# Kernel tuning notes

Hardware: AMD Instinct MI355X
Metric: run time of the kernel (lower is better)

## Reference

```python
import jax, jax.numpy as jnp
import numpy as np

B, T = 16, 2048
P_DIM = 512
NC = 8          # num_codebooks
CS = 256        # codebook_size
HD = 256        # hidden_dim (must equal CS, see module structure)
TOT = NC * CS   # 2048
SELF_OUT = (NC - 1) * HD
SELF_IN = (NC - 1) * CS
EPS = 1e-5


def setup_inputs() -> dict:
    key = jax.random.key(0)
    ks = jax.random.split(key, 6)
    predictor = jax.random.normal(ks[0], (B, T, P_DIM), dtype=jnp.float32)
    codebook_indexes = jax.random.randint(ks[1], (B, T, NC), 0, CS, dtype=jnp.int32)
    # linear1: predictor_dim -> NC*HD
    W1 = jax.random.normal(ks[2], (NC * HD, P_DIM), dtype=jnp.float32) * P_DIM ** -0.5
    b1 = jnp.zeros((NC * HD,), jnp.float32)
    # linear_self parameter, init as in the module
    linear_self = jax.random.normal(ks[3], (SELF_OUT, SELF_IN), dtype=jnp.float32) * SELF_IN ** -0.5
    # LayerNorm affine params
    gamma = jnp.ones((TOT,), jnp.float32)
    beta = jnp.zeros((TOT,), jnp.float32)
    # linear2: NC*HD -> NC*CS
    W2 = jax.random.normal(ks[4], (TOT, NC * HD), dtype=jnp.float32) * (NC * HD) ** -0.5
    b2 = jnp.zeros((TOT,), jnp.float32)
    return {"predictor": predictor, "codebook_indexes": codebook_indexes,
            "W1": W1, "b1": b1, "linear_self": linear_self,
            "gamma": gamma, "beta": beta, "W2": W2, "b2": b2}


def _self_mask():
    # block lower-triangular (inclusive) mask: out block i sees in blocks <= i
    oi = jnp.arange(SELF_OUT) // HD
    ii = jnp.arange(SELF_IN) // CS
    return (oi[:, None] >= ii[None, :]).astype(jnp.float32)


def reference(predictor, codebook_indexes, W1, b1, linear_self, gamma, beta, W2, b2):
    idx = codebook_indexes.astype(jnp.int32)
    N = idx.shape[0] * idx.shape[1]
    idx_f = idx.reshape(N, NC)
    pred_f = predictor.reshape(N, P_DIM)

    cb_mask = idx_f >= 0                                   # [N, NC]
    idx_floor = jnp.maximum(idx_f, 0)
    # scatter one-hot exactly as torch scatter_ (no per-codebook offset)
    one_hot = jnp.zeros((N, TOT), jnp.float32).at[
        jnp.arange(N)[:, None], idx_floor].set(cb_mask.astype(jnp.float32))

    one_hot_part = one_hot[:, : TOT - CS]                  # [N, (NC-1)*CS]
    W_self = linear_self * _self_mask()                    # [(NC-1)*HD, (NC-1)*CS]
    self_pred = one_hot_part @ W_self.T                    # [N, (NC-1)*HD]

    hidden = pred_f @ W1.T + b1                            # [N, NC*HD]
    hidden = hidden.at[:, CS:].add(self_pred)

    h = jax.nn.relu(hidden)
    mu = jnp.mean(h, axis=-1, keepdims=True)
    var = jnp.mean(jnp.square(h - mu), axis=-1, keepdims=True)
    h = (h - mu) * jax.lax.rsqrt(var + EPS) * gamma + beta

    logits = h @ W2.T + b2                                 # [N, TOT]
    logprobs = jax.nn.log_softmax(logits.reshape(N, NC, CS), axis=-1).reshape(N, TOT)

    tot_logprob = jnp.vdot(logprobs, one_hot)
    tot_count = jnp.sum(cb_mask)
    return tot_logprob, tot_count
```

## Files before the change

kernel.cpp:

```cpp
#include <hip/hip_runtime.h>

#define NROWS 32768
#define PD    512
#define NCB   8
#define CSZ   256
#define TOTD  2048
#define SIN   1792

typedef float floatx4  __attribute__((ext_vector_type(4)));
typedef float floatx16 __attribute__((ext_vector_type(16)));
typedef int   intx4    __attribute__((ext_vector_type(4)));
typedef int   intx8    __attribute__((ext_vector_type(8)));

__device__ __forceinline__ float bf2f(unsigned int h) {
    return __uint_as_float(h << 16);
}
__device__ __forceinline__ unsigned short f2bf(float f) {
    unsigned int u = __float_as_uint(f);
    u += 0x7FFFu + ((u >> 16) & 1u);
    return (unsigned short)(u >> 16);
}
__device__ __forceinline__ unsigned char f2fp8(float v) {
    int p = __builtin_amdgcn_cvt_pk_fp8_f32(v, v, 0, false);
    return (unsigned char)(p & 0xFF);
}

__device__ __forceinline__ void gload16(const unsigned char* g, unsigned char* l) {
    __builtin_amdgcn_global_load_lds(
        (const __attribute__((address_space(1))) void*)g,
        (__attribute__((address_space(3))) void*)l, 16, 0, 0);
}

#define MFMA64(ACC, A, B)                                                     \
    asm volatile("v_mfma_f32_32x32x64_f8f6f4 %0, %1, %2, %0"                  \
                 : "+a"(ACC) : "v"(A), "v"(B))

__global__ __launch_bounds__(256) void k_cvt8(const float* __restrict__ in,
                                              unsigned char* __restrict__ out,
                                              float scale, int n8) {
    int i = blockIdx.x * 256 + threadIdx.x;
    if (i >= n8) return;
    float4 a = ((const float4*)in)[2 * i];
    float4 b = ((const float4*)in)[2 * i + 1];
    int p0 = __builtin_amdgcn_cvt_pk_fp8_f32(a.x * scale, a.y * scale, 0, false);
    p0     = __builtin_amdgcn_cvt_pk_fp8_f32(a.z * scale, a.w * scale, p0, true);
    int p1 = __builtin_amdgcn_cvt_pk_fp8_f32(b.x * scale, b.y * scale, 0, false);
    p1     = __builtin_amdgcn_cvt_pk_fp8_f32(b.z * scale, b.w * scale, p1, true);
    int2 o; o.x = p0; o.y = p1;
    ((int2*)out)[i] = o;
}

__global__ __launch_bounds__(256) void k_tb(const float* __restrict__ in,
                                            unsigned short* __restrict__ out) {
    __shared__ float t[32][33];
    int bx = blockIdx.x * 32, by = blockIdx.y * 32;
    int tx = threadIdx.x & 31, ty = threadIdx.x >> 5;
#pragma unroll
    for (int j = 0; j < 32; j += 8)
        t[ty + j][tx] = in[(size_t)(by + ty + j) * SIN + bx + tx];
    __syncthreads();
#pragma unroll
    for (int j = 0; j < 32; j += 8)
        out[(size_t)(bx + ty + j) * SIN + by + tx] = f2bf(t[tx][ty + j]);
}


__global__ __launch_bounds__(512)
void k_gemm1(const unsigned char* __restrict__ A,
             const unsigned char* __restrict__ Bw,
             const float* __restrict__ bias,
             unsigned char* __restrict__ Out) {
    const int K = PD;
    __shared__ __align__(16) unsigned char As[3 * 8192];
    __shared__ __align__(16) unsigned char Bs[3 * 8192];

    const int tid  = threadIdx.x;
    const int lane = tid & 63;
    const int wave = tid >> 6;
    const int wm = (wave >> 2) << 6;
    const int wn = (wave & 3) << 5;
    const int bid  = blockIdx.x;
    const int row0 = (bid & 255) << 7;
    const int col0 = (bid >> 8) << 7;

    floatx16 acc0 = 0.f, acc1 = 0.f;

    const int gran  = lane >> 1;
    const int srow  = ((wave >> 1) << 5) + (gran ^ ((gran & 12) >> 2));
    const int skoff = ((wave & 1) << 5) + ((lane & 1) << 4);
    const unsigned char* Ag = A  + (size_t)(row0 + srow) * K + skoff;
    const unsigned char* Bg = Bw + (size_t)(col0 + srow) * K + skoff;
    unsigned char* Al = As + wave * 1024;
    unsigned char* Bl = Bs + wave * 1024;

    gload16(Ag,      Al);
    gload16(Bg,      Bl);
    gload16(Ag + 64, Al + 8192);
    gload16(Bg + 64, Bl + 8192);

    const int ro = (lane << 5) ^ ((lane & 12) << 3);
    const int aoff = (wave >> 2) << 12;
    const int boff = (wave & 3) << 11;

    auto compute = [&](int cbuf) {
        const unsigned char* Ab = As + cbuf * 8192 + aoff + ro;
        const unsigned char* Bb = Bs + cbuf * 8192 + boff + ro;
        intx8 a0 = *(const intx8*)Ab;
        intx8 a1 = *(const intx8*)(Ab + 2048);
        intx8 b0 = *(const intx8*)Bb;
        MFMA64(acc0, a0, b0);
        MFMA64(acc1, a1, b0);
    };

    const int NI = K / 64;
    int cb = 0, nb = 2;
    for (int i = 0; i < NI - 1; ++i) {
        asm volatile("s_waitcnt vmcnt(2)" ::: "memory");
        asm volatile("s_barrier" ::: "memory");
        if (i + 2 < NI) {
            const int k0 = (i + 2) * 64;
            gload16(Ag + k0, Al + nb * 8192);
            gload16(Bg + k0, Bl + nb * 8192);
        }
        compute(cb);
        cb = (cb + 1 == 3) ? 0 : cb + 1;
        nb = (nb + 1 == 3) ? 0 : nb + 1;
    }
    asm volatile("s_waitcnt vmcnt(0)" ::: "memory");
    asm volatile("s_barrier" ::: "memory");
    compute(cb);
    asm volatile("s_nop 7\n\ts_nop 7\n\ts_nop 7" ::: "memory");

    const int l31  = lane & 31;
    const int half = lane >> 5;
    const int col  = col0 + wn + l31;
    const float bcol = bias[col];
#pragma unroll
    for (int r = 0; r < 16; ++r) {
        const int rl = (r & 3) + ((r >> 2) << 3) + (half << 2);
        Out[(size_t)(row0 + wm + rl) * TOTD + col]      = f2fp8((acc0[r] * 0.0625f + bcol) * 8.f);
        Out[(size_t)(row0 + wm + 32 + rl) * TOTD + col] = f2fp8((acc1[r] * 0.0625f + bcol) * 8.f);
    }
}

__global__ __launch_bounds__(256) void k_ln(const unsigned char* __restrict__ Hraw8,
                                            unsigned char* __restrict__ H8,
                                            const unsigned short* __restrict__ LSTb,
                                            const int* __restrict__ idx,
                                            const float* __restrict__ gamma,
                                            const float* __restrict__ beta) {
    const int row = blockIdx.x;
    const int tid = threadIdx.x;
    __shared__ int sidx[8];
    __shared__ float ws4[4], wss4[4];
    if (tid < 8) sidx[tid] = idx[(size_t)row * NCB + tid];

    uint2 w = ((const uint2*)(Hraw8 + (size_t)row * TOTD))[tid];
    float x[8];
    x[0] = __builtin_amdgcn_cvt_f32_fp8(w.x, 0) * 0.125f;
    x[1] = __builtin_amdgcn_cvt_f32_fp8(w.x, 1) * 0.125f;
    x[2] = __builtin_amdgcn_cvt_f32_fp8(w.x, 2) * 0.125f;
    x[3] = __builtin_amdgcn_cvt_f32_fp8(w.x, 3) * 0.125f;
    x[4] = __builtin_amdgcn_cvt_f32_fp8(w.y, 0) * 0.125f;
    x[5] = __builtin_amdgcn_cvt_f32_fp8(w.y, 1) * 0.125f;
    x[6] = __builtin_amdgcn_cvt_f32_fp8(w.y, 2) * 0.125f;
    x[7] = __builtin_amdgcn_cvt_f32_fp8(w.y, 3) * 0.125f;
    __syncthreads();

    const int gt = tid >> 5;
#pragma unroll
    for (int c = 0; c < 7; ++c) {
        if (c < gt) {
            int ic = sidx[c];
            if (ic >= 0) {
                uint4 v = *(const uint4*)(LSTb + (size_t)(c * CSZ + ic) * SIN + (tid * 8 - CSZ));
                x[0] += bf2f(v.x & 0xFFFF); x[1] += bf2f(v.x >> 16);
                x[2] += bf2f(v.y & 0xFFFF); x[3] += bf2f(v.y >> 16);
                x[4] += bf2f(v.z & 0xFFFF); x[5] += bf2f(v.z >> 16);
                x[6] += bf2f(v.w & 0xFFFF); x[7] += bf2f(v.w >> 16);
            }
        }
    }
#pragma unroll
    for (int e = 0; e < 8; ++e) x[e] = fmaxf(x[e], 0.f);

    float s = 0.f, ss = 0.f;
#pragma unroll
    for (int e = 0; e < 8; ++e) { s += x[e]; ss += x[e] * x[e]; }
#pragma unroll
    for (int o = 32; o; o >>= 1) { s += __shfl_xor(s, o); ss += __shfl_xor(ss, o); }
    if ((tid & 63) == 0) { ws4[tid >> 6] = s; wss4[tid >> 6] = ss; }
    __syncthreads();
    s  = ws4[0] + ws4[1] + ws4[2] + ws4[3];
    ss = wss4[0] + wss4[1] + wss4[2] + wss4[3];
    const float mu = s * (1.f / TOTD);
    const float var = ss * (1.f / TOTD) - mu * mu;
    const float rstd = rsqrtf(var + 1e-5f);
    float y[8];
#pragma unroll
    for (int e = 0; e < 8; ++e) {
        int col = tid * 8 + e;
        y[e] = ((x[e] - mu) * rstd * gamma[col] + beta[col]) * 8.f;
    }
    int p0 = __builtin_amdgcn_cvt_pk_fp8_f32(y[0], y[1], 0, false);
    p0     = __builtin_amdgcn_cvt_pk_fp8_f32(y[2], y[3], p0, true);
    int p1 = __builtin_amdgcn_cvt_pk_fp8_f32(y[4], y[5], 0, false);
    p1     = __builtin_amdgcn_cvt_pk_fp8_f32(y[6], y[7], p1, true);
    int2 o; o.x = p0; o.y = p1;
    ((int2*)(H8 + (size_t)row * TOTD))[tid] = o;
}

__global__ __launch_bounds__(512)
void k_gemm2(const unsigned char* __restrict__ H,
             const unsigned char* __restrict__ W2,
             const float* __restrict__ b2,
             const int* __restrict__ idx,
             float* __restrict__ pm_,
             float* __restrict__ ps_,
             float* __restrict__ pt_) {
    const int K = TOTD;
    __shared__ __align__(16) unsigned char As[3 * 8192];
    __shared__ __align__(16) unsigned char Bs[3 * 8192];
    __shared__ int tidx[128];

    const int tid  = threadIdx.x;
    const int lane = tid & 63;
    const int wave = tid >> 6;
    const int wm = (wave >> 2) << 6;
    const int wn = (wave & 3) << 5;
    const int bid  = blockIdx.x;
    const int row0 = (bid & 255) << 7;
    const int col0 = (bid >> 8) << 7;
    const int g    = col0 >> 8;

    floatx16 acc0 = 0.f, acc1 = 0.f;

    const int gran  = lane >> 1;
    const int srow  = ((wave >> 1) << 5) + (gran ^ ((gran & 12) >> 2));
    const int skoff = ((wave & 1) << 5) + ((lane & 1) << 4);
    const unsigned char* Ag = H  + (size_t)(row0 + srow) * K + skoff;
    const unsigned char* Bg = W2 + (size_t)(col0 + srow) * K + skoff;
    unsigned char* Al = As + wave * 1024;
    unsigned char* Bl = Bs + wave * 1024;

    if (tid < 128) tidx[tid] = idx[(size_t)(row0 + tid) * NCB + g];

    gload16(Ag,      Al);
    gload16(Bg,      Bl);
    gload16(Ag + 64, Al + 8192);
    gload16(Bg + 64, Bl + 8192);

    const int ro = (lane << 5) ^ ((lane & 12) << 3);
    const int aoff = (wave >> 2) << 12;
    const int boff = (wave & 3) << 11;

    auto compute = [&](int cbuf) {
        const unsigned char* Ab = As + cbuf * 8192 + aoff + ro;
        const unsigned char* Bb = Bs + cbuf * 8192 + boff + ro;
        intx8 a0 = *(const intx8*)Ab;
        intx8 a1 = *(const intx8*)(Ab + 2048);
        intx8 b0 = *(const intx8*)Bb;
        MFMA64(acc0, a0, b0);
        MFMA64(acc1, a1, b0);
    };

    const int NI = K / 64;
    int cb = 0, nb = 2;
    for (int i = 0; i < NI - 1; ++i) {
        asm volatile("s_waitcnt vmcnt(2)" ::: "memory");
        asm volatile("s_barrier" ::: "memory");
        if (i + 2 < NI) {
            const int k0 = (i + 2) * 64;
            gload16(Ag + k0, Al + nb * 8192);
            gload16(Bg + k0, Bl + nb * 8192);
        }
        compute(cb);
        cb = (cb + 1 == 3) ? 0 : cb + 1;
        nb = (nb + 1 == 3) ? 0 : nb + 1;
    }
    asm volatile("s_waitcnt vmcnt(0)" ::: "memory");
    asm volatile("s_barrier" ::: "memory");
    compute(cb);
    asm volatile("s_nop 7\n\ts_nop 7\n\ts_nop 7" ::: "memory");

    const int l31  = lane & 31;
    const int half = lane >> 5;
    const int slot = (col0 + wn) >> 5;
    const int coff = (col0 & 255) + wn;
    const float bc = b2[col0 + wn + l31];

    auto epi = [&](const floatx16& A0, int mtoff) {
#pragma unroll
        for (int r = 0; r < 16; ++r) {
            const int lrow = wm + mtoff + (r & 3) + ((r >> 2) << 3) + (half << 2);
            const int ic   = tidx[lrow];
            const int tloc = ic - coff;
            float v = A0[r] * 0.0078125f + bc;
            float mm = v;
            float tv = (ic >= 0 && l31 == tloc) ? v : 0.f;
#pragma unroll
            for (int o = 1; o < 32; o <<= 1) mm = fmaxf(mm, __shfl_xor(mm, o));
            float sv = __expf(v - mm);
#pragma unroll
            for (int o = 1; o < 32; o <<= 1) { sv += __shfl_xor(sv, o); tv += __shfl_xor(tv, o); }
            if (l31 == 0) {
                const int row = row0 + lrow;
                pm_[(size_t)slot * NROWS + row] = mm;
                ps_[(size_t)slot * NROWS + row] = sv;
                pt_[(size_t)slot * NROWS + row] = tv;
            }
        }
    };
    epi(acc0, 0);
    epi(acc1, 32);
}

__global__ __launch_bounds__(256) void k_comb(const float* __restrict__ pm_,
                                              const float* __restrict__ ps_,
                                              const float* __restrict__ pt_,
                                              const int* __restrict__ idx,
                                              float* __restrict__ out) {
    const int i   = blockIdx.x * 256 + threadIdx.x;
    const int row = i & (NROWS - 1);
    const int g   = i >> 15;
    const int ic  = idx[(size_t)row * NCB + g];
    float lp = 0.f, cnt = 0.f;
    if (ic >= 0) {
        const size_t b = (size_t)(g * 8) * NROWS + row;
        float m[8], s[8], t = 0.f;
        float mm = -3.4e38f;
#pragma unroll
        for (int k = 0; k < 8; ++k) {
            m[k] = pm_[b + (size_t)k * NROWS];
            s[k] = ps_[b + (size_t)k * NROWS];
            t   += pt_[b + (size_t)k * NROWS];
            mm = fmaxf(mm, m[k]);
        }
        float Z = 0.f;
#pragma unroll
        for (int k = 0; k < 8; ++k) Z += s[k] * __expf(m[k] - mm);
        lp = t - (mm + __logf(Z));
        cnt = 1.f;
    }
#pragma unroll
    for (int o = 1; o < 64; o <<= 1) { lp += __shfl_xor(lp, o); cnt += __shfl_xor(cnt, o); }
    __shared__ float wred[8];
    const int lane = threadIdx.x & 63, wave = threadIdx.x >> 6;
    if (lane == 0) { wred[wave] = lp; wred[4 + wave] = cnt; }
    __syncthreads();
    if (threadIdx.x == 0) {
        atomicAdd(&out[0], wred[0] + wred[1] + wred[2] + wred[3]);
        atomicAdd(&out[1], wred[4] + wred[5] + wred[6] + wred[7]);
    }
}

extern "C" void kernel_launch(void* const* d_in, const int* in_sizes, int n_in,
                              void* d_out, int out_size, void* d_ws, size_t ws_size,
                              hipStream_t stream) {
    const float* predictor = (const float*)d_in[0];
    const int*   cbidx     = (const int*)d_in[1];
    const float* W1        = (const float*)d_in[2];
    const float* b1        = (const float*)d_in[3];
    const float* LS        = (const float*)d_in[4];
    const float* gamma     = (const float*)d_in[5];
    const float* beta      = (const float*)d_in[6];
    const float* W2        = (const float*)d_in[7];
    const float* b2        = (const float*)d_in[8];
    float* out = (float*)d_out;

    char* ws = (char*)d_ws;
    size_t off = 0;
    auto alloc = [&](size_t bytes) {
        char* p = ws + off;
        off += (bytes + 255) & ~(size_t)255;
        return p;
    };
    unsigned char* Hraw8 = (unsigned char*)alloc((size_t)NROWS * TOTD);
    unsigned char* R2    = (unsigned char*)alloc((size_t)NROWS * TOTD);
    unsigned char* W2_8  = (unsigned char*)alloc((size_t)TOTD * TOTD);
    unsigned short* LSTb = (unsigned short*)alloc((size_t)SIN * SIN * 2);

    unsigned char* pred8 = R2;
    unsigned char* W1_8  = R2 + (size_t)NROWS * PD;
    unsigned char* H8    = R2;
    float* pm_ = (float*)Hraw8;
    float* ps_ = pm_ + (size_t)64 * NROWS;
    float* pt_ = ps_ + (size_t)64 * NROWS;

    hipMemsetAsync(d_out, 0, 2 * sizeof(float), stream);

    k_cvt8<<<NROWS * PD / 8 / 256, 256, 0, stream>>>(predictor, pred8, 1.f, NROWS * PD / 8);
    k_cvt8<<<TOTD * PD / 8 / 256, 256, 0, stream>>>(W1, W1_8, 16.f, TOTD * PD / 8);
    k_cvt8<<<TOTD * TOTD / 8 / 256, 256, 0, stream>>>(W2, W2_8, 16.f, TOTD * TOTD / 8);
    k_tb<<<dim3(SIN / 32, SIN / 32), 256, 0, stream>>>(LS, LSTb);

    k_gemm1<<<16 * 256, 512, 0, stream>>>(pred8, W1_8, b1, Hraw8);
    k_ln<<<NROWS, 256, 0, stream>>>(Hraw8, H8, LSTb, cbidx, gamma, beta);
    k_gemm2<<<16 * 256, 512, 0, stream>>>(H8, W2_8, b2, cbidx, pm_, ps_, pt_);
    k_comb<<<NROWS * NCB / 256, 256, 0, stream>>>(pm_, ps_, pt_, cbidx, out);
}
```

Measured before the change: 592.4 us.

## Enlarge FP8 GEMM tiles to 256x128 with 4 waves and swizzled block order

Both FP8 GEMMs move from 128x128 tiles with 8 waves (2 MFMAs per wave per k-step) to 256x128 tiles with 4 waves, each computing a 128x64 sub-tile with 8 accumulators. This raises arithmetic intensity per LDS and global load and cuts the number of blocks. A block-index swizzle groups blocks that share the same B columns to improve L2 reuse. The costs are higher register pressure, more LDS per block (72KB), and fewer waves to hide latency.

```diff
diff --git a/kernel.cpp b/kernel.cpp
--- a/kernel.cpp
+++ b/kernel.cpp
@@ -34,6 +34,8 @@
 #define MFMA64(ACC, A, B)                                                     \
     asm volatile("v_mfma_f32_32x32x64_f8f6f4 %0, %1, %2, %0"                  \
                  : "+a"(ACC) : "v"(A), "v"(B))
+
+#define SBAR() asm volatile("s_barrier" ::: "memory")
 
 __global__ __launch_bounds__(256) void k_cvt8(const float* __restrict__ in,
                                               unsigned char* __restrict__ out,
@@ -65,82 +67,94 @@
 }
 
 
-__global__ __launch_bounds__(512)
+__global__ __launch_bounds__(256)
 void k_gemm1(const unsigned char* __restrict__ A,
              const unsigned char* __restrict__ Bw,
              const float* __restrict__ bias,
              unsigned char* __restrict__ Out) {
     const int K = PD;
-    __shared__ __align__(16) unsigned char As[3 * 8192];
-    __shared__ __align__(16) unsigned char Bs[3 * 8192];
+    __shared__ __align__(16) unsigned char S[3 * 24576];
 
     const int tid  = threadIdx.x;
     const int lane = tid & 63;
-    const int wave = tid >> 6;
-    const int wm = (wave >> 2) << 6;
-    const int wn = (wave & 3) << 5;
-    const int bid  = blockIdx.x;
-    const int row0 = (bid & 255) << 7;
-    const int col0 = (bid >> 8) << 7;
-
-    floatx16 acc0 = 0.f, acc1 = 0.f;
-
-    const int gran  = lane >> 1;
-    const int srow  = ((wave >> 1) << 5) + (gran ^ ((gran & 12) >> 2));
-    const int skoff = ((wave & 1) << 5) + ((lane & 1) << 4);
-    const unsigned char* Ag = A  + (size_t)(row0 + srow) * K + skoff;
-    const unsigned char* Bg = Bw + (size_t)(col0 + srow) * K + skoff;
-    unsigned char* Al = As + wave * 1024;
-    unsigned char* Bl = Bs + wave * 1024;
-
-    gload16(Ag,      Al);
-    gload16(Bg,      Bl);
-    gload16(Ag + 64, Al + 8192);
-    gload16(Bg + 64, Bl + 8192);
+    const int w    = tid >> 6;
+    const int wm   = (w >> 1) << 7;
+    const int wn   = (w & 1) << 6;
+    const int swz  = (blockIdx.x & 7) * 256 + (blockIdx.x >> 3);
+    const int row0 = (swz & 127) << 8;
+    const int col0 = (swz >> 7) << 7;
+
+    floatx16 a00 = 0.f, a01 = 0.f, a10 = 0.f, a11 = 0.f;
+    floatx16 a20 = 0.f, a21 = 0.f, a30 = 0.f, a31 = 0.f;
+
+    const int gran = lane >> 1;
+    const int sig  = gran ^ ((gran & 12) >> 2);
+    const unsigned char* Ag = A  + (size_t)(row0 + (w << 6) + sig) * K + ((lane & 1) << 4);
+    const unsigned char* Bg = Bw + (size_t)(col0 + (w << 5) + sig) * K + ((lane & 1) << 4);
+
+    auto stage = [&](int buf, int k0) {
+        unsigned char* d = S + buf * 24576;
+        gload16(Ag + k0,              d + (w << 12));
+        gload16(Ag + k0 + 32,         d + (w << 12) + 1024);
+        gload16(Ag + k0 + 32 * K,     d + (w << 12) + 2048);
+        gload16(Ag + k0 + 32 * K + 32,d + (w << 12) + 3072);
+        gload16(Bg + k0,              d + 16384 + (w << 11));
+        gload16(Bg + k0 + 32,         d + 16384 + (w << 11) + 1024);
+    };
 
     const int ro = (lane << 5) ^ ((lane & 12) << 3);
-    const int aoff = (wave >> 2) << 12;
-    const int boff = (wave & 3) << 11;
 
     auto compute = [&](int cbuf) {
-        const unsigned char* Ab = As + cbuf * 8192 + aoff + ro;
-        const unsigned char* Bb = Bs + cbuf * 8192 + boff + ro;
-        intx8 a0 = *(const intx8*)Ab;
-        intx8 a1 = *(const intx8*)(Ab + 2048);
-        intx8 b0 = *(const intx8*)Bb;
-        MFMA64(acc0, a0, b0);
-        MFMA64(acc1, a1, b0);
-    };
+        const unsigned char* base = S + cbuf * 24576;
+        const unsigned char* Ab = base + ((w >> 1) << 13) + ro;
+        const unsigned char* Bb = base + 16384 + ((w & 1) << 12) + ro;
+        intx8 A0 = *(const intx8*)Ab;
+        intx8 A1 = *(const intx8*)(Ab + 2048);
+        intx8 A2 = *(const intx8*)(Ab + 4096);
+        intx8 A3 = *(const intx8*)(Ab + 6144);
+        intx8 B0 = *(const intx8*)Bb;
+        intx8 B1 = *(const intx8*)(Bb + 2048);
+        MFMA64(a00, A0, B0); MFMA64(a01, A0, B1);
+        MFMA64(a10, A1, B0); MFMA64(a11, A1, B1);
+        MFMA64(a20, A2, B0); MFMA64(a21, A2, B1);
+        MFMA64(a30, A3, B0); MFMA64(a31, A3, B1);
+    };
+
+    stage(0, 0);
+    stage(1, 64);
 
     const int NI = K / 64;
     int cb = 0, nb = 2;
     for (int i = 0; i < NI - 1; ++i) {
-        asm volatile("s_waitcnt vmcnt(2)" ::: "memory");
-        asm volatile("s_barrier" ::: "memory");
-        if (i + 2 < NI) {
-            const int k0 = (i + 2) * 64;
-            gload16(Ag + k0, Al + nb * 8192);
-            gload16(Bg + k0, Bl + nb * 8192);
-        }
+        asm volatile("s_waitcnt vmcnt(6)" ::: "memory");
+        SBAR();
+        if (i + 2 < NI) stage(nb, (i + 2) * 64);
         compute(cb);
         cb = (cb + 1 == 3) ? 0 : cb + 1;
         nb = (nb + 1 == 3) ? 0 : nb + 1;
     }
     asm volatile("s_waitcnt vmcnt(0)" ::: "memory");
-    asm volatile("s_barrier" ::: "memory");
+    SBAR();
     compute(cb);
     asm volatile("s_nop 7\n\ts_nop 7\n\ts_nop 7" ::: "memory");
 
     const int l31  = lane & 31;
     const int half = lane >> 5;
-    const int col  = col0 + wn + l31;
-    const float bcol = bias[col];
-#pragma unroll
-    for (int r = 0; r < 16; ++r) {
-        const int rl = (r & 3) + ((r >> 2) << 3) + (half << 2);
-        Out[(size_t)(row0 + wm + rl) * TOTD + col]      = f2fp8((acc0[r] * 0.0625f + bcol) * 8.f);
-        Out[(size_t)(row0 + wm + 32 + rl) * TOTD + col] = f2fp8((acc1[r] * 0.0625f + bcol) * 8.f);
-    }
+    const float bc0 = bias[col0 + wn + l31];
+    const float bc1 = bias[col0 + wn + 32 + l31];
+    auto epi = [&](const floatx16& Aa, const floatx16& Ab2, int jrow) {
+        const int col = col0 + wn + l31;
+#pragma unroll
+        for (int r = 0; r < 16; ++r) {
+            const int row = row0 + wm + jrow + (r & 3) + ((r >> 2) << 3) + (half << 2);
+            Out[(size_t)row * TOTD + col]      = f2fp8((Aa[r]  * 0.0625f + bc0) * 8.f);
+            Out[(size_t)row * TOTD + col + 32] = f2fp8((Ab2[r] * 0.0625f + bc1) * 8.f);
+        }
+    };
+    epi(a00, a01, 0);
+    epi(a10, a11, 32);
+    epi(a20, a21, 64);
+    epi(a30, a31, 96);
 }
 
 __global__ __launch_bounds__(256) void k_ln(const unsigned char* __restrict__ Hraw8,
@@ -210,7 +224,7 @@
     ((int2*)(H8 + (size_t)row * TOTD))[tid] = o;
 }
 
-__global__ __launch_bounds__(512)
+__global__ __launch_bounds__(256)
 void k_gemm2(const unsigned char* __restrict__ H,
              const unsigned char* __restrict__ W2,
              const float* __restrict__ b2,
@@ -219,85 +233,90 @@
              float* __restrict__ ps_,
              float* __restrict__ pt_) {
     const int K = TOTD;
-    __shared__ __align__(16) unsigned char As[3 * 8192];
-    __shared__ __align__(16) unsigned char Bs[3 * 8192];
-    __shared__ int tidx[128];
+    __shared__ __align__(16) unsigned char S[3 * 24576];
+    __shared__ int tidx[256];
 
     const int tid  = threadIdx.x;
     const int lane = tid & 63;
-    const int wave = tid >> 6;
-    const int wm = (wave >> 2) << 6;
-    const int wn = (wave & 3) << 5;
-    const int bid  = blockIdx.x;
-    const int row0 = (bid & 255) << 7;
-    const int col0 = (bid >> 8) << 7;
+    const int w    = tid >> 6;
+    const int wm   = (w >> 1) << 7;
+    const int wn   = (w & 1) << 6;
+    const int swz  = (blockIdx.x & 7) * 256 + (blockIdx.x >> 3);
+    const int row0 = (swz & 127) << 8;
+    const int col0 = (swz >> 7) << 7;
     const int g    = col0 >> 8;
 
-    floatx16 acc0 = 0.f, acc1 = 0.f;
-
-    const int gran  = lane >> 1;
-    const int srow  = ((wave >> 1) << 5) + (gran ^ ((gran & 12) >> 2));
-    const int skoff = ((wave & 1) << 5) + ((lane & 1) << 4);
-    const unsigned char* Ag = H  + (size_t)(row0 + srow) * K + skoff;
-    const unsigned char* Bg = W2 + (size_t)(col0 + srow) * K + skoff;
-    unsigned char* Al = As + wave * 1024;
-    unsigned char* Bl = Bs + wave * 1024;
-
-    if (tid < 128) tidx[tid] = idx[(size_t)(row0 + tid) * NCB + g];
-
-    gload16(Ag,      Al);
-    gload16(Bg,      Bl);
-    gload16(Ag + 64, Al + 8192);
-    gload16(Bg + 64, Bl + 8192);
+    floatx16 a00 = 0.f, a01 = 0.f, a10 = 0.f, a11 = 0.f;
+    floatx16 a20 = 0.f, a21 = 0.f, a30 = 0.f, a31 = 0.f;
+
+    tidx[tid] = idx[(size_t)(row0 + tid) * NCB + g];
+
+    const int gran = lane >> 1;
+    const int sig  = gran ^ ((gran & 12) >> 2);
+    const unsigned char* Ag = H  + (size_t)(row0 + (w << 6) + sig) * K + ((lane & 1) << 4);
+    const unsigned char* Bg = W2 + (size_t)(col0 + (w << 5) + sig) * K + ((lane & 1) << 4);
+
+    auto stage = [&](int buf, int k0) {
+        unsigned char* d = S + buf * 24576;
+        gload16(Ag + k0,               d + (w << 12));
+        gload16(Ag + k0 + 32,          d + (w << 12) + 1024);
+        gload16(Ag + k0 + 32 * K,      d + (w << 12) + 2048);
+        gload16(Ag + k0 + 32 * K + 32, d + (w << 12) + 3072);
+        gload16(Bg + k0,               d + 16384 + (w << 11));
+        gload16(Bg + k0 + 32,          d + 16384 + (w << 11) + 1024);
+    };
 
     const int ro = (lane << 5) ^ ((lane & 12) << 3);
-    const int aoff = (wave >> 2) << 12;
-    const int boff = (wave & 3) << 11;
 
     auto compute = [&](int cbuf) {
-        const unsigned char* Ab = As + cbuf * 8192 + aoff + ro;
-        const unsigned char* Bb = Bs + cbuf * 8192 + boff + ro;
-        intx8 a0 = *(const intx8*)Ab;
-        intx8 a1 = *(const intx8*)(Ab + 2048);
-        intx8 b0 = *(const intx8*)Bb;
-        MFMA64(acc0, a0, b0);
-        MFMA64(acc1, a1, b0);
-    };
+        const unsigned char* base = S + cbuf * 24576;
+        const unsigned char* Ab = base + ((w >> 1) << 13) + ro;
+        const unsigned char* Bb = base + 16384 + ((w & 1) << 12) + ro;
+        intx8 A0 = *(const intx8*)Ab;
+        intx8 A1 = *(const intx8*)(Ab + 2048);
+        intx8 A2 = *(const intx8*)(Ab + 4096);
+        intx8 A3 = *(const intx8*)(Ab + 6144);
+        intx8 B0 = *(const intx8*)Bb;
+        intx8 B1 = *(const intx8*)(Bb + 2048);
+        MFMA64(a00, A0, B0); MFMA64(a01, A0, B1);
+        MFMA64(a10, A1, B0); MFMA64(a11, A1, B1);
+        MFMA64(a20, A2, B0); MFMA64(a21, A2, B1);
+        MFMA64(a30, A3, B0); MFMA64(a31, A3, B1);
+    };
+
+    stage(0, 0);
+    stage(1, 64);
 
     const int NI = K / 64;
     int cb = 0, nb = 2;
     for (int i = 0; i < NI - 1; ++i) {
-        asm volatile("s_waitcnt vmcnt(2)" ::: "memory");
-        asm volatile("s_barrier" ::: "memory");
-        if (i + 2 < NI) {
-            const int k0 = (i + 2) * 64;
-            gload16(Ag + k0, Al + nb * 8192);
-            gload16(Bg + k0, Bl + nb * 8192);
-        }
+        asm volatile("s_waitcnt vmcnt(6)" ::: "memory");
+        SBAR();
+        if (i + 2 < NI) stage(nb, (i + 2) * 64);
         compute(cb);
         cb = (cb + 1 == 3) ? 0 : cb + 1;
         nb = (nb + 1 == 3) ? 0 : nb + 1;
     }
     asm volatile("s_waitcnt vmcnt(0)" ::: "memory");
-    asm volatile("s_barrier" ::: "memory");
+    SBAR();
     compute(cb);
     asm volatile("s_nop 7\n\ts_nop 7\n\ts_nop 7" ::: "memory");
 
     const int l31  = lane & 31;
     const int half = lane >> 5;
-    const int slot = (col0 + wn) >> 5;
+    const int slotbase = (col0 + wn) >> 5;
     const int coff = (col0 & 255) + wn;
-    const float bc = b2[col0 + wn + l31];
-
-    auto epi = [&](const floatx16& A0, int mtoff) {
+    const float bc0 = b2[col0 + wn + l31];
+    const float bc1 = b2[col0 + wn + 32 + l31];
+
+    auto epi = [&](const floatx16& Aa, int jrow, int kk, float bc) {
 #pragma unroll
         for (int r = 0; r < 16; ++r) {
-            const int lrow = wm + mtoff + (r & 3) + ((r >> 2) << 3) + (half << 2);
+            const int lrow = wm + jrow + (r & 3) + ((r >> 2) << 3) + (half << 2);
             const int ic   = tidx[lrow];
-            const int tloc = ic - coff;
-            float v = A0[r] * 0.0078125f + bc;
+            float v = Aa[r] * 0.0078125f + bc;
             float mm = v;
-            float tv = (ic >= 0 && l31 == tloc) ? v : 0.f;
+            float tv = (ic >= 0 && l31 == ic - coff - (kk << 5)) ? v : 0.f;
 #pragma unroll
             for (int o = 1; o < 32; o <<= 1) mm = fmaxf(mm, __shfl_xor(mm, o));
             float sv = __expf(v - mm);
@@ -305,14 +324,16 @@
             for (int o = 1; o < 32; o <<= 1) { sv += __shfl_xor(sv, o); tv += __shfl_xor(tv, o); }
             if (l31 == 0) {
                 const int row = row0 + lrow;
-                pm_[(size_t)slot * NROWS + row] = mm;
-                ps_[(size_t)slot * NROWS + row] = sv;
-                pt_[(size_t)slot * NROWS + row] = tv;
+                pm_[(size_t)(slotbase + kk) * NROWS + row] = mm;
+                ps_[(size_t)(slotbase + kk) * NROWS + row] = sv;
+                pt_[(size_t)(slotbase + kk) * NROWS + row] = tv;
             }
         }
     };
-    epi(acc0, 0);
-    epi(acc1, 32);
+    epi(a00, 0, 0, bc0);  epi(a01, 0, 1, bc1);
+    epi(a10, 32, 0, bc0); epi(a11, 32, 1, bc1);
+    epi(a20, 64, 0, bc0); epi(a21, 64, 1, bc1);
+    epi(a30, 96, 0, bc0); epi(a31, 96, 1, bc1);
 }
 
 __global__ __launch_bounds__(256) void k_comb(const float* __restrict__ pm_,
@@ -394,8 +415,8 @@
     k_cvt8<<<TOTD * TOTD / 8 / 256, 256, 0, stream>>>(W2, W2_8, 16.f, TOTD * TOTD / 8);
     k_tb<<<dim3(SIN / 32, SIN / 32), 256, 0, stream>>>(LS, LSTb);
 
-    k_gemm1<<<16 * 256, 512, 0, stream>>>(pred8, W1_8, b1, Hraw8);
+    k_gemm1<<<2048, 256, 0, stream>>>(pred8, W1_8, b1, Hraw8);
     k_ln<<<NROWS, 256, 0, stream>>>(Hraw8, H8, LSTb, cbidx, gamma, beta);
-    k_gemm2<<<16 * 256, 512, 0, stream>>>(H8, W2_8, b2, cbidx, pm_, ps_, pt_);
+    k_gemm2<<<2048, 256, 0, stream>>>(H8, W2_8, b2, cbidx, pm_, ps_, pt_);
     k_comb<<<NROWS * NCB / 256, 256, 0, stream>>>(pm_, ps_, pt_, cbidx, out);
 }
```

Measured after the change: 682.7 us. 15.3% more time.
